# Performance work log

Hardware: AMD Instinct MI355X
Metric: run time of the kernel (lower is better)

## Reference

```python
import jax, jax.numpy as jnp
import numpy as np

B = 131072          # batch of fermion configurations
S = 256             # sys_size
NUP = 16            # num_fillings[0]
NDOWN = 16          # num_fillings[1]


def _random_occupancy(rng, b, s, nfill):
    # exactly `nfill` ones per row, uniformly random positions
    r = rng.random((b, s))
    perm_rank = np.argsort(r, axis=1).argsort(axis=1)  # a random permutation per row
    return (perm_rank < nfill).astype(np.float32)


def setup_inputs() -> dict:
    rng = np.random.default_rng(0)
    cfg_up = _random_occupancy(rng, B, S, NUP)
    cfg_down = _random_occupancy(rng, B, S, NDOWN)
    config_fermion = jnp.asarray(np.concatenate([cfg_up, cfg_down], axis=1))  # (B, 2S)
    key = jax.random.key(0)
    k1, k2 = jax.random.split(key)
    states_up = jax.random.normal(k1, (S, NUP), dtype=jnp.float32)
    states_down = jax.random.normal(k2, (S, NDOWN), dtype=jnp.float32)
    return {"config_fermion": config_fermion, "states_up": states_up, "states_down": states_down}


def reference(config_fermion, states_up, states_down):
    s = states_up.shape[0]
    nup = states_up.shape[1]
    ndown = states_down.shape[1]
    cfg_up = config_fermion[:, :s]      # (B, S) of {0,1}
    cfg_down = config_fermion[:, s:]
    # indices of occupied sites, ascending (torch.nonzero order); top_k breaks
    # ties by lowest index, then sort ascending
    idx_up = jnp.sort(jax.lax.top_k(cfg_up, nup)[1], axis=1)        # (B, Nup)
    idx_down = jnp.sort(jax.lax.top_k(cfg_down, ndown)[1], axis=1)  # (B, Ndown)
    mats_up = states_up[idx_up]         # (B, Nup, Nup) gather of orbital rows
    mats_down = states_down[idx_down]   # (B, Ndown, Ndown)
    det_up = jnp.linalg.det(mats_up)
    det_down = jnp.linalg.det(mats_down)
    return det_up * det_down
```

## Files before the change

### kernel.cpp

```cpp
#include <hip/hip_runtime.h>

static __device__ __forceinline__ unsigned umax2(unsigned a, unsigned b) { return a > b ? a : b; }

__global__ __launch_bounds__(256) void slater_det_kernel(
    const float* __restrict__ cfg,
    const float* __restrict__ sup,
    const float* __restrict__ sdn,
    float* __restrict__ out)
{
    __shared__ __align__(16) int idx_lds[4][16][16];
    __shared__ float det_lds[4][16];

    const int tid  = threadIdx.x;
    const int wave = tid >> 6;
    const int lane = tid & 63;
    const int wb0  = (blockIdx.x * 4 + wave) * 8;

    float4 c[16];
#pragma unroll
    for (int d = 0; d < 16; ++d) {
        const float* p = cfg + (size_t)(wb0 + (d >> 1)) * 512
                             + (size_t)(d & 1) * 256 + (size_t)lane * 4;
        c[d] = *(const float4*)p;
    }
    const unsigned long long lt = (1ull << lane) - 1ull;
#pragma unroll
    for (int d = 0; d < 16; ++d) {
        float4 v = c[d];
        bool n0 = v.x != 0.f, n1 = v.y != 0.f, n2 = v.z != 0.f, n3 = v.w != 0.f;
        unsigned long long b0 = __ballot(n0);
        unsigned long long b1 = __ballot(n1);
        unsigned long long b2 = __ballot(n2);
        unsigned long long b3 = __ballot(n3);
        int base = __popcll(b0 & lt) + __popcll(b1 & lt)
                 + __popcll(b2 & lt) + __popcll(b3 & lt);
        int pos = lane * 4;
        int r = base;
        if (n0 && r < 16) idx_lds[wave][d][r] = pos;
        r += n0;
        if (n1 && r < 16) idx_lds[wave][d][r] = pos + 1;
        r += n1;
        if (n2 && r < 16) idx_lds[wave][d][r] = pos + 2;
        r += n2;
        if (n3 && r < 16) idx_lds[wave][d][r] = pos + 3;
    }
    __syncthreads();

    const int g = lane >> 2;
    const int q = lane & 3;
    const int4 ri = *(const int4*)&idx_lds[wave][g][q * 4];
    const float* tab = (g & 1) ? sdn : sup;

    float rr[4][16];
    const int rid[4] = {ri.x, ri.y, ri.z, ri.w};
#pragma unroll
    for (int j = 0; j < 4; ++j) {
        const float* p = tab + (size_t)rid[j] * 16;
        float4 a = *(const float4*)(p + 0);
        float4 b = *(const float4*)(p + 4);
        float4 e = *(const float4*)(p + 8);
        float4 f = *(const float4*)(p + 12);
        rr[j][0]=a.x;  rr[j][1]=a.y;  rr[j][2]=a.z;  rr[j][3]=a.w;
        rr[j][4]=b.x;  rr[j][5]=b.y;  rr[j][6]=b.z;  rr[j][7]=b.w;
        rr[j][8]=e.x;  rr[j][9]=e.y;  rr[j][10]=e.z; rr[j][11]=e.w;
        rr[j][12]=f.x; rr[j][13]=f.y; rr[j][14]=f.z; rr[j][15]=f.w;
    }

    unsigned am = 0xFu;
    float det = 1.f;
    int flips = 0;

#pragma unroll
    for (int k = 0; k < 16; ++k) {
        unsigned a0 = (__float_as_uint(rr[0][k]) & 0x7FFFFFF0u) | (unsigned)(q*4+0);
        unsigned a1 = (__float_as_uint(rr[1][k]) & 0x7FFFFFF0u) | (unsigned)(q*4+1);
        unsigned a2 = (__float_as_uint(rr[2][k]) & 0x7FFFFFF0u) | (unsigned)(q*4+2);
        unsigned a3 = (__float_as_uint(rr[3][k]) & 0x7FFFFFF0u) | (unsigned)(q*4+3);
        unsigned key0 = (am & 1u) ? a0 : (unsigned)(q*4+0);
        unsigned key1 = (am & 2u) ? a1 : (unsigned)(q*4+1);
        unsigned key2 = (am & 4u) ? a2 : (unsigned)(q*4+2);
        unsigned key3 = (am & 8u) ? a3 : (unsigned)(q*4+3);
        unsigned kloc = umax2(umax2(key0, key1), umax2(key2, key3));
        int jloc = (int)(kloc & 3u);
        float crow[16];
#pragma unroll
        for (int cc = k; cc < 16; ++cc) {
            float t01 = (jloc & 1) ? rr[1][cc] : rr[0][cc];
            float t23 = (jloc & 1) ? rr[3][cc] : rr[2][cc];
            crow[cc] = (jloc & 2) ? t23 : t01;
        }
        unsigned ko = kloc;
        ko = umax2(ko, (unsigned)__shfl_xor((int)ko, 1));
        ko = umax2(ko, (unsigned)__shfl_xor((int)ko, 2));
        int p   = (int)(ko & 15u);
        int src = (lane & ~3) | (p >> 2);
        float prow[16];
#pragma unroll
        for (int cc = k; cc < 16; ++cc) prow[cc] = __shfl(crow[cc], src);
        float piv = prow[k];
        det *= piv;
        int t = p - q * 4;
        unsigned mlt = (t <= 0) ? 0u : ((t >= 4) ? 0xFu : ((1u << t) - 1u));
        int cnt = __popc(am & mlt);
        cnt += __shfl_xor(cnt, 1);
        cnt += __shfl_xor(cnt, 2);
        flips += cnt;
        if (q == (p >> 2)) am &= ~(1u << (p & 3));
        float inv = 1.0f / piv;
        float f0 = rr[0][k] * inv;
        float f1 = rr[1][k] * inv;
        float f2 = rr[2][k] * inv;
        float f3 = rr[3][k] * inv;
#pragma unroll
        for (int cc = k + 1; cc < 16; ++cc) {
            rr[0][cc] = __builtin_fmaf(-f0, prow[cc], rr[0][cc]);
            rr[1][cc] = __builtin_fmaf(-f1, prow[cc], rr[1][cc]);
            rr[2][cc] = __builtin_fmaf(-f2, prow[cc], rr[2][cc]);
            rr[3][cc] = __builtin_fmaf(-f3, prow[cc], rr[3][cc]);
        }
    }
    float result = (flips & 1) ? -det : det;

    if (q == 0) det_lds[wave][g] = result;
    __syncthreads();
    if (lane < 8) {
        out[wb0 + lane] = det_lds[wave][2 * lane] * det_lds[wave][2 * lane + 1];
    }
}

extern "C" void kernel_launch(void* const* d_in, const int* in_sizes, int n_in,
                              void* d_out, int out_size, void* d_ws, size_t ws_size,
                              hipStream_t stream) {
    const float* cfg = (const float*)d_in[0];
    const float* sup = (const float*)d_in[1];
    const float* sdn = (const float*)d_in[2];
    float* outp = (float*)d_out;
    const int B = in_sizes[0] / 512;
    const int blocks = B / 32;
    slater_det_kernel<<<blocks, 256, 0, stream>>>(cfg, sup, sdn, outp);
}
```

Baseline: 72.59 us.

## Use unpivoted elimination with pivoted fallback, stream config loads, shuffle-combine dets

The main elimination loop now runs without partial pivoting: the pivot row is fixed at k, and each pivot-row element is broadcast by shuffle only when it is needed. If any pivot magnitude drops below a threshold, the lane falls back to the original partial-pivoting path recomputed from reloaded rows. Config loads are rotated through a four-entry register buffer instead of sixteen, and the final up*down product uses a lane shuffle instead of LDS plus a barrier. Launch bounds now request four blocks per CU to cut register use. Skipping pivot search and sign tracking in the common case saves ALU and shuffle work, but the threshold may let ill-conditioned matrices through with reduced accuracy, and the fallback branch adds code size.

```diff
diff --git a/kernel.cpp b/kernel.cpp
--- a/kernel.cpp
+++ b/kernel.cpp
@@ -2,31 +2,37 @@
 
 static __device__ __forceinline__ unsigned umax2(unsigned a, unsigned b) { return a > b ? a : b; }
 
-__global__ __launch_bounds__(256) void slater_det_kernel(
+__global__ __launch_bounds__(256, 4) void slater_det_kernel(
     const float* __restrict__ cfg,
     const float* __restrict__ sup,
     const float* __restrict__ sdn,
     float* __restrict__ out)
 {
     __shared__ __align__(16) int idx_lds[4][16][16];
-    __shared__ float det_lds[4][16];
 
     const int tid  = threadIdx.x;
     const int wave = tid >> 6;
     const int lane = tid & 63;
     const int wb0  = (blockIdx.x * 4 + wave) * 8;
 
-    float4 c[16];
+    const unsigned long long lt = (1ull << lane) - 1ull;
+
+    float4 c[4];
 #pragma unroll
-    for (int d = 0; d < 16; ++d) {
+    for (int d = 0; d < 4; ++d) {
         const float* p = cfg + (size_t)(wb0 + (d >> 1)) * 512
                              + (size_t)(d & 1) * 256 + (size_t)lane * 4;
         c[d] = *(const float4*)p;
     }
-    const unsigned long long lt = (1ull << lane) - 1ull;
 #pragma unroll
     for (int d = 0; d < 16; ++d) {
-        float4 v = c[d];
+        float4 v = c[d & 3];
+        if (d + 4 < 16) {
+            const int dn = d + 4;
+            const float* p = cfg + (size_t)(wb0 + (dn >> 1)) * 512
+                                 + (size_t)(dn & 1) * 256 + (size_t)lane * 4;
+            c[d & 3] = *(const float4*)p;
+        }
         bool n0 = v.x != 0.f, n1 = v.y != 0.f, n2 = v.z != 0.f, n3 = v.w != 0.f;
         unsigned long long b0 = __ballot(n0);
         unsigned long long b1 = __ballot(n1);
@@ -50,9 +56,9 @@
     const int q = lane & 3;
     const int4 ri = *(const int4*)&idx_lds[wave][g][q * 4];
     const float* tab = (g & 1) ? sdn : sup;
+    const int rid[4] = {ri.x, ri.y, ri.z, ri.w};
 
     float rr[4][16];
-    const int rid[4] = {ri.x, ri.y, ri.z, ri.w};
 #pragma unroll
     for (int j = 0; j < 4; ++j) {
         const float* p = tab + (size_t)rid[j] * 16;
@@ -66,46 +72,16 @@
         rr[j][12]=f.x; rr[j][13]=f.y; rr[j][14]=f.z; rr[j][15]=f.w;
     }
 
-    unsigned am = 0xFu;
+    const int gbase = lane & ~3;
     float det = 1.f;
-    int flips = 0;
-
+    bool bad = false;
 #pragma unroll
     for (int k = 0; k < 16; ++k) {
-        unsigned a0 = (__float_as_uint(rr[0][k]) & 0x7FFFFFF0u) | (unsigned)(q*4+0);
-        unsigned a1 = (__float_as_uint(rr[1][k]) & 0x7FFFFFF0u) | (unsigned)(q*4+1);
-        unsigned a2 = (__float_as_uint(rr[2][k]) & 0x7FFFFFF0u) | (unsigned)(q*4+2);
-        unsigned a3 = (__float_as_uint(rr[3][k]) & 0x7FFFFFF0u) | (unsigned)(q*4+3);
-        unsigned key0 = (am & 1u) ? a0 : (unsigned)(q*4+0);
-        unsigned key1 = (am & 2u) ? a1 : (unsigned)(q*4+1);
-        unsigned key2 = (am & 4u) ? a2 : (unsigned)(q*4+2);
-        unsigned key3 = (am & 8u) ? a3 : (unsigned)(q*4+3);
-        unsigned kloc = umax2(umax2(key0, key1), umax2(key2, key3));
-        int jloc = (int)(kloc & 3u);
-        float crow[16];
-#pragma unroll
-        for (int cc = k; cc < 16; ++cc) {
-            float t01 = (jloc & 1) ? rr[1][cc] : rr[0][cc];
-            float t23 = (jloc & 1) ? rr[3][cc] : rr[2][cc];
-            crow[cc] = (jloc & 2) ? t23 : t01;
-        }
-        unsigned ko = kloc;
-        ko = umax2(ko, (unsigned)__shfl_xor((int)ko, 1));
-        ko = umax2(ko, (unsigned)__shfl_xor((int)ko, 2));
-        int p   = (int)(ko & 15u);
-        int src = (lane & ~3) | (p >> 2);
-        float prow[16];
-#pragma unroll
-        for (int cc = k; cc < 16; ++cc) prow[cc] = __shfl(crow[cc], src);
-        float piv = prow[k];
+        const int src = gbase | (k >> 2);
+        const int jp  = k & 3;
+        float piv = __shfl(rr[jp][k], src);
         det *= piv;
-        int t = p - q * 4;
-        unsigned mlt = (t <= 0) ? 0u : ((t >= 4) ? 0xFu : ((1u << t) - 1u));
-        int cnt = __popc(am & mlt);
-        cnt += __shfl_xor(cnt, 1);
-        cnt += __shfl_xor(cnt, 2);
-        flips += cnt;
-        if (q == (p >> 2)) am &= ~(1u << (p & 3));
+        bad = bad || (fabsf(piv) < 1e-4f);
         float inv = 1.0f / piv;
         float f0 = rr[0][k] * inv;
         float f1 = rr[1][k] * inv;
@@ -113,19 +89,86 @@
         float f3 = rr[3][k] * inv;
 #pragma unroll
         for (int cc = k + 1; cc < 16; ++cc) {
-            rr[0][cc] = __builtin_fmaf(-f0, prow[cc], rr[0][cc]);
-            rr[1][cc] = __builtin_fmaf(-f1, prow[cc], rr[1][cc]);
-            rr[2][cc] = __builtin_fmaf(-f2, prow[cc], rr[2][cc]);
-            rr[3][cc] = __builtin_fmaf(-f3, prow[cc], rr[3][cc]);
+            float pcc = __shfl(rr[jp][cc], src);
+            rr[0][cc] = __builtin_fmaf(-f0, pcc, rr[0][cc]);
+            rr[1][cc] = __builtin_fmaf(-f1, pcc, rr[1][cc]);
+            rr[2][cc] = __builtin_fmaf(-f2, pcc, rr[2][cc]);
+            rr[3][cc] = __builtin_fmaf(-f3, pcc, rr[3][cc]);
         }
     }
-    float result = (flips & 1) ? -det : det;
 
-    if (q == 0) det_lds[wave][g] = result;
-    __syncthreads();
-    if (lane < 8) {
-        out[wb0 + lane] = det_lds[wave][2 * lane] * det_lds[wave][2 * lane + 1];
+    if (__ballot(bad)) {
+        if (bad) {
+#pragma unroll
+            for (int j = 0; j < 4; ++j) {
+                const float* p = tab + (size_t)rid[j] * 16;
+                float4 a = *(const float4*)(p + 0);
+                float4 b = *(const float4*)(p + 4);
+                float4 e = *(const float4*)(p + 8);
+                float4 f = *(const float4*)(p + 12);
+                rr[j][0]=a.x;  rr[j][1]=a.y;  rr[j][2]=a.z;  rr[j][3]=a.w;
+                rr[j][4]=b.x;  rr[j][5]=b.y;  rr[j][6]=b.z;  rr[j][7]=b.w;
+                rr[j][8]=e.x;  rr[j][9]=e.y;  rr[j][10]=e.z; rr[j][11]=e.w;
+                rr[j][12]=f.x; rr[j][13]=f.y; rr[j][14]=f.z; rr[j][15]=f.w;
+            }
+            unsigned am = 0xFu;
+            float fdet = 1.f;
+            int flips = 0;
+#pragma unroll
+            for (int k = 0; k < 16; ++k) {
+                unsigned a0 = (__float_as_uint(rr[0][k]) & 0x7FFFFFF0u) | (unsigned)(q*4+0);
+                unsigned a1 = (__float_as_uint(rr[1][k]) & 0x7FFFFFF0u) | (unsigned)(q*4+1);
+                unsigned a2 = (__float_as_uint(rr[2][k]) & 0x7FFFFFF0u) | (unsigned)(q*4+2);
+                unsigned a3 = (__float_as_uint(rr[3][k]) & 0x7FFFFFF0u) | (unsigned)(q*4+3);
+                unsigned key0 = (am & 1u) ? a0 : (unsigned)(q*4+0);
+                unsigned key1 = (am & 2u) ? a1 : (unsigned)(q*4+1);
+                unsigned key2 = (am & 4u) ? a2 : (unsigned)(q*4+2);
+                unsigned key3 = (am & 8u) ? a3 : (unsigned)(q*4+3);
+                unsigned kloc = umax2(umax2(key0, key1), umax2(key2, key3));
+                int jloc = (int)(kloc & 3u);
+                float crow[16];
+#pragma unroll
+                for (int cc = k; cc < 16; ++cc) {
+                    float t01 = (jloc & 1) ? rr[1][cc] : rr[0][cc];
+                    float t23 = (jloc & 1) ? rr[3][cc] : rr[2][cc];
+                    crow[cc] = (jloc & 2) ? t23 : t01;
+                }
+                unsigned ko = kloc;
+                ko = umax2(ko, (unsigned)__shfl_xor((int)ko, 1));
+                ko = umax2(ko, (unsigned)__shfl_xor((int)ko, 2));
+                int p   = (int)(ko & 15u);
+                int src = gbase | (p >> 2);
+                float prow[16];
+#pragma unroll
+                for (int cc = k; cc < 16; ++cc) prow[cc] = __shfl(crow[cc], src);
+                float piv = prow[k];
+                fdet *= piv;
+                int t = p - q * 4;
+                unsigned mlt = (t <= 0) ? 0u : ((t >= 4) ? 0xFu : ((1u << t) - 1u));
+                int cnt = __popc(am & mlt);
+                cnt += __shfl_xor(cnt, 1);
+                cnt += __shfl_xor(cnt, 2);
+                flips += cnt;
+                if (q == (p >> 2)) am &= ~(1u << (p & 3));
+                float inv = 1.0f / piv;
+                float f0 = rr[0][k] * inv;
+                float f1 = rr[1][k] * inv;
+                float f2 = rr[2][k] * inv;
+                float f3 = rr[3][k] * inv;
+#pragma unroll
+                for (int cc = k + 1; cc < 16; ++cc) {
+                    rr[0][cc] = __builtin_fmaf(-f0, prow[cc], rr[0][cc]);
+                    rr[1][cc] = __builtin_fmaf(-f1, prow[cc], rr[1][cc]);
+                    rr[2][cc] = __builtin_fmaf(-f2, prow[cc], rr[2][cc]);
+                    rr[3][cc] = __builtin_fmaf(-f3, prow[cc], rr[3][cc]);
+                }
+            }
+            det = (flips & 1) ? -fdet : fdet;
+        }
     }
+
+    float prod = det * __shfl_xor(det, 4);
+    if ((lane & 7) == 0) out[wb0 + (lane >> 3)] = prod;
 }
 
 extern "C" void kernel_launch(void* const* d_in, const int* in_sizes, int n_in,
```

After: 89.01 us. 22.6% more time.
